# Performance work log

Hardware: AMD Instinct MI355X
Metric: run time of the kernel (lower is better)

## Reference

```python
import jax, jax.numpy as jnp
import numpy as np
import math

N_EMBD = 1024
N_HEAD_DIM = 64
B, S = 8, 2048

def setup_inputs() -> dict:
    key = jax.random.key(0)
    ks = jax.random.split(key, 8)
    x = jax.random.normal(ks[0], (B, S, N_EMBD), dtype=jnp.float32)
    padding_mask = jax.random.randint(ks[1], (B, S), 0, 2).astype(jnp.bool_)
    scale = 1.0 / math.sqrt(N_EMBD)
    Wq = jax.random.normal(ks[2], (N_HEAD_DIM, N_EMBD), dtype=jnp.float32) * scale
    bq = jnp.zeros((N_HEAD_DIM,), dtype=jnp.float32)
    Wk = jax.random.normal(ks[3], (N_HEAD_DIM, N_EMBD), dtype=jnp.float32) * scale
    bk = jnp.zeros((N_HEAD_DIM,), dtype=jnp.float32)
    Wv = jax.random.normal(ks[4], (N_HEAD_DIM, N_EMBD), dtype=jnp.float32) * scale
    bv = jnp.zeros((N_HEAD_DIM,), dtype=jnp.float32)
    return {"x": x, "Wq": Wq, "bq": bq, "Wk": Wk, "bk": bk, "Wv": Wv, "bv": bv,
            "padding_mask": padding_mask}

def reference(x, Wq, bq, Wk, bk, Wv, bv, padding_mask):
    # q,k,v: [B,S,D] via Linear (x @ W^T + b)
    q = jnp.einsum('bse,de->bsd', x, Wq) + bq
    k = jnp.einsum('bse,de->bsd', x, Wk) + bk
    v = jnp.einsum('bse,de->bsd', x, Wv) + bv
    scale = 1.0 / math.sqrt(k.shape[-1])
    att = jnp.einsum('bqd,bkd->bqk', q, k) * scale  # [B,S,S]
    # padding_mask [B,S] -> [B,1,S]: True positions masked to -inf
    att = jnp.where(padding_mask[:, None, :], -jnp.inf, att)
    att = jax.nn.softmax(att, axis=-1)
    # attn_dropout omitted (eval mode / identity)
    return jnp.einsum('bqk,bkd->bqd', att, v)
```

## Files before the change

kernel.cpp:

```cpp
#include <hip/hip_runtime.h>
#include <hip/hip_bf16.h>

#define B_ 8
#define S_ 2048
#define E_ 1024
#define D_ 64
#define VT_STRIDE 2112

typedef short short8 __attribute__((ext_vector_type(8)));
typedef short short4v __attribute__((ext_vector_type(4)));
typedef float floatx4 __attribute__((ext_vector_type(4)));

static __device__ __forceinline__ short bf16_bits(float f) {
    __hip_bfloat16 h = __float2bfloat16(f);
    return *reinterpret_cast<short*>(&h);
}
static __device__ __forceinline__ float bits_to_f(short s) {
    __hip_bfloat16 h = *reinterpret_cast<__hip_bfloat16*>(&s);
    return __bfloat162float(h);
}
static __device__ __forceinline__ void split8(const float* __restrict__ p,
                                              short8& hi, short8& lo) {
    #pragma unroll
    for (int j = 0; j < 8; j++) {
        float f = p[j];
        short h = bf16_bits(f);
        hi[j] = h;
        lo[j] = bf16_bits(f - bits_to_f(h));
    }
}
static __device__ __forceinline__ void split8v(const float v[8],
                                               short8& hi, short8& lo) {
    #pragma unroll
    for (int j = 0; j < 8; j++) {
        float f = v[j];
        short h = bf16_bits(f);
        hi[j] = h;
        lo[j] = bf16_bits(f - bits_to_f(h));
    }
}
static __device__ __forceinline__ void dma16(const void* src, void* lds_dst) {
    __builtin_amdgcn_global_load_lds(
        (const __attribute__((address_space(1))) unsigned int*)src,
        (__attribute__((address_space(3))) unsigned int*)lds_dst, 16, 0, 0);
}

__global__ __launch_bounds__(256) void prep_kernel(
    const float* __restrict__ Wq, const float* __restrict__ Wk,
    const float* __restrict__ Wv, short8* __restrict__ Wpk8,
    const void* __restrict__ mask_raw, float* __restrict__ maskf)
{
    __shared__ unsigned int red[256];
    if (blockIdx.x < 96) {
        const int t = blockIdx.x * 256 + threadIdx.x;
        const int l16  = t & 15;
        const int quad = (t >> 4) & 3;
        const int nb   = (t >> 6) & 3;
        const int m    = (t >> 8) % 3;
        const int e0c  = (t >> 8) / 3;
        const float* W = (m == 0) ? Wq : ((m == 1) ? Wk : Wv);
        short8 hi, lo;
        split8(W + (size_t)(nb * 16 + l16) * E_ + e0c * 32 + quad * 8, hi, lo);
        Wpk8[(size_t)e0c * 768 + m * 256 + nb * 64 + quad * 16 + l16] = hi;
    } else {
        const unsigned int* w = (const unsigned int*)mask_raw;
        unsigned int local = 0;
        for (int i = threadIdx.x; i < 4096; i += 256) local |= w[i];
        red[threadIdx.x] = local;
        __syncthreads();
        for (int s = 128; s > 0; s >>= 1) {
            if (threadIdx.x < s) red[threadIdx.x] |= red[threadIdx.x + s];
            __syncthreads();
        }
        const unsigned int ov = red[0];
        const bool is_u8 = (ov > 1u) && ((ov >> 24) <= 1u);
        const int i = (blockIdx.x - 96) * 256 + threadIdx.x;
        int v;
        if (ov == 0u)      v = 0;
        else if (is_u8)    v = (int)((const unsigned char*)mask_raw)[i];
        else               v = (((const unsigned int*)mask_raw)[i] != 0u);
        maskf[i] = v ? -1e30f : 0.0f;
    }
}

__global__ __launch_bounds__(512, 4) void qkv_kernel(
    const float* __restrict__ x, const short8* __restrict__ Wpk8,
    const float* __restrict__ bq, const float* __restrict__ bk,
    const float* __restrict__ bv,
    short* __restrict__ Qhi, short* __restrict__ Qlo,
    short* __restrict__ Khi, short* __restrict__ Vt)
{
    __shared__ alignas(16) float  xs[2][2][1024];
    __shared__ alignas(16) short8 wt[2][1536];
    const int tid  = threadIdx.x;
    const int wave = tid >> 6;
    const int nb   = wave & 3;
    const int rt   = wave >> 2;
    const int lane = tid & 63;
    const int l16  = lane & 15;
    const int quad = lane >> 4;
    const int row0 = blockIdx.x * 32;

    const int xr_  = (tid >> 3) & 31;
    const int xc_  = tid >> 8;
    const float* xsrc = x + (size_t)(row0 + xr_) * E_ + xc_ * 32 +
                        (((tid & 7) ^ (xr_ & 7)) * 4);
    const int xdst = xc_ * 1024 + xr_ * 32 + (tid & 7) * 4;

    floatx4 acc[3];
    #pragma unroll
    for (int m = 0; m < 3; m++) acc[m] = (floatx4){0.f,0.f,0.f,0.f};

    #pragma unroll
    for (int i = 0; i < 3; i++)
        dma16(Wpk8 + (size_t)i * 512 + tid, &wt[0][i * 512 + tid]);
    dma16(xsrc, &xs[0][0][0] + xdst);

    int buf = 0;
    for (int R = 0; R < 16; ++R) {
        __syncthreads();
        if (R + 1 < 16) {
            #pragma unroll
            for (int i = 0; i < 3; i++)
                dma16(Wpk8 + (size_t)(R + 1) * 1536 + i * 512 + tid,
                      &wt[buf ^ 1][i * 512 + tid]);
            dma16(xsrc + (R + 1) * 64, &xs[buf ^ 1][0][0] + xdst);
        }

        #pragma unroll
        for (int c = 0; c < 2; c++) {
            const int rr = rt * 16 + l16;
            const int rx = rr & 7;
            const float* xrp = &xs[buf][c][rr * 32];
            float4 a0 = *reinterpret_cast<const float4*>(xrp + (((2 * quad)     ^ rx) * 4));
            float4 a1 = *reinterpret_cast<const float4*>(xrp + (((2 * quad + 1) ^ rx) * 4));
            float av[8] = {a0.x, a0.y, a0.z, a0.w, a1.x, a1.y, a1.z, a1.w};
            short8 ah, al;
            split8v(av, ah, al);
            #pragma unroll
            for (int m = 0; m < 3; m++) {
                short8 wh = wt[buf][c * 768 + m * 256 + nb * 64 + lane];
                acc[m] = __builtin_amdgcn_mfma_f32_16x16x32_bf16(al, wh, acc[m], 0, 0, 0);
                acc[m] = __builtin_amdgcn_mfma_f32_16x16x32_bf16(ah, wh, acc[m], 0, 0, 0);
            }
        }
        buf ^= 1;
    }

    const int d = nb * 16 + l16;
    const float bqv = bq[d];
    const float bkv = bk[d];
    const float bvv = bv[d];
    const int bch = row0 >> 11;
    const int rowbase = row0 + rt * 16 + quad * 4;
    short4v vpk;
    #pragma unroll
    for (int r = 0; r < 4; r++) {
        const size_t row = (size_t)(rowbase + r);
        const float q = (acc[0][r] + bqv) * 0.125f;
        const short qhv = bf16_bits(q);
        Qhi[row * 64 + d] = qhv;
        Qlo[row * 64 + d] = bf16_bits(q - bits_to_f(qhv));
        Khi[row * 64 + d] = bf16_bits(acc[1][r] + bkv);
        vpk[r] = bf16_bits(acc[2][r] + bvv);
    }
    *reinterpret_cast<short4v*>(Vt + ((size_t)(bch * 64 + d)) * VT_STRIDE +
                                (rowbase & 2047)) = vpk;
}

union alignas(16) AttnLds {
    struct { short8 kts[4][512]; short8 vts[4][512]; } st;
    struct {
        float Osh[4][16][65];
        float msh[4][16], lsh[4][16];
    } mg;
};

__global__ __launch_bounds__(256, 2) void attn_kernel(
    const short* __restrict__ Qhi, const short* __restrict__ Qlo,
    const short* __restrict__ Khi, const short* __restrict__ Vt,
    const float* __restrict__ maskf, float* __restrict__ out)
{
    __shared__ AttnLds lds;
    __shared__ short PlT[4][16][72];

    const int tid  = threadIdx.x;
    const int wave = tid >> 6;
    const int qsub = wave & 1;
    const int par  = wave >> 1;
    const int lane = tid & 63;
    const int l16  = lane & 15;
    const int quad = lane >> 4;
    const int b    = blockIdx.x >> 6;
    const int qt   = blockIdx.x & 63;
    const size_t qbase  = (size_t)b * S_ + qt * 32 + qsub * 16;
    const size_t kplane = (size_t)b * S_;
    const short* Vb = Vt + (size_t)b * 64 * VT_STRIDE;

    short8 qh[2], ql[2];
    #pragma unroll
    for (int dc = 0; dc < 2; dc++) {
        qh[dc] = *reinterpret_cast<const short8*>(Qhi + (qbase + l16) * 64 + dc * 32 + quad * 8);
        ql[dc] = *reinterpret_cast<const short8*>(Qlo + (qbase + l16) * 64 + dc * 32 + quad * 8);
    }

    float m = -1e30f, l = 0.f;
    floatx4 O[4];
    #pragma unroll
    for (int ob = 0; ob < 4; ob++) O[ob] = (floatx4){0.f,0.f,0.f,0.f};

    #pragma unroll
    for (int p = 0; p < 2; p++) {
        #pragma unroll
        for (int i = 0; i < 2; i++) {
            const int c = i * 256 + tid;
            const int r = c >> 3, cs = c & 7;
            dma16(Khi + (kplane + p * 64 + r) * 64 + ((cs ^ (r & 7)) * 8),
                  &lds.st.kts[p][c]);
            dma16(Vb + (size_t)r * VT_STRIDE + p * 64 + ((cs ^ (r & 7)) * 8),
                  &lds.st.vts[p][c]);
        }
    }
    float4 mk4[4];
    #pragma unroll
    for (int kb = 0; kb < 4; kb++)
        mk4[kb] = *reinterpret_cast<const float4*>(
            maskf + kplane + par * 64 + kb * 16 + quad * 4);

    for (int R = 0; R < 16; ++R) {
        __syncthreads();
        const int set = R & 1;
        if (R + 1 < 16) {
            const int nset = set ^ 1;
            const int kt2 = (R + 1) * 128;
            #pragma unroll
            for (int p = 0; p < 2; p++) {
                #pragma unroll
                for (int i = 0; i < 2; i++) {
                    const int c = i * 256 + tid;
                    const int r = c >> 3, cs = c & 7;
                    dma16(Khi + (kplane + kt2 + p * 64 + r) * 64 + ((cs ^ (r & 7)) * 8),
                          &lds.st.kts[nset * 2 + p][c]);
                    dma16(Vb + (size_t)r * VT_STRIDE + kt2 + p * 64 + ((cs ^ (r & 7)) * 8),
                          &lds.st.vts[nset * 2 + p][c]);
                }
            }
        }
        const int buf = set * 2 + par;

        floatx4 sc[4];
        #pragma unroll
        for (int kb = 0; kb < 4; kb++) {
            floatx4 a = (floatx4){0.f,0.f,0.f,0.f};
            #pragma unroll
            for (int kc = 0; kc < 2; kc++) {
                const int key = kb * 16 + l16;
                short8 kf = lds.st.kts[buf][key * 8 + ((kc * 4 + quad) ^ (key & 7))];
                a = __builtin_amdgcn_mfma_f32_16x16x32_bf16(kf, qh[kc], a, 0, 0, 0);
                a = __builtin_amdgcn_mfma_f32_16x16x32_bf16(kf, ql[kc], a, 0, 0, 0);
            }
            sc[kb] = a;
        }
        #pragma unroll
        for (int kb = 0; kb < 4; kb++) {
            const float* mkp = reinterpret_cast<const float*>(&mk4[kb]);
            #pragma unroll
            for (int r = 0; r < 4; r++) sc[kb][r] += mkp[r];
        }

        if (R + 1 < 16) {
            const int ktn = (R + 1) * 128 + par * 64;
            #pragma unroll
            for (int kb = 0; kb < 4; kb++)
                mk4[kb] = *reinterpret_cast<const float4*>(
                    maskf + kplane + ktn + kb * 16 + quad * 4);
        }

        float mx = -1e30f;
        #pragma unroll
        for (int kb = 0; kb < 4; kb++)
            #pragma unroll
            for (int r = 0; r < 4; r++) mx = fmaxf(mx, sc[kb][r]);
        mx = fmaxf(mx, __shfl_xor(mx, 16, 64));
        mx = fmaxf(mx, __shfl_xor(mx, 32, 64));
        const float mnew  = fmaxf(fmaxf(m, mx), -1e29f);
        const float alpha = __expf(m - mnew);
        float ps = 0.f;
        #pragma unroll
        for (int kb = 0; kb < 4; kb++)
            #pragma unroll
            for (int r = 0; r < 4; r++) {
                const float pe = __expf(sc[kb][r] - mnew);
                sc[kb][r] = pe;
                ps += pe;
            }
        ps += __shfl_xor(ps, 16, 64);
        ps += __shfl_xor(ps, 32, 64);
        l = l * alpha + ps;
        m = mnew;
        #pragma unroll
        for (int ob = 0; ob < 4; ob++) O[ob] *= alpha;

        #pragma unroll
        for (int kb = 0; kb < 4; kb++)
            #pragma unroll
            for (int r = 0; r < 4; r++)
                PlT[wave][l16][kb * 16 + quad * 4 + r] = bf16_bits(sc[kb][r]);
        short8 pf[2];
        #pragma unroll
        for (int kc = 0; kc < 2; kc++)
            pf[kc] = *reinterpret_cast<const short8*>(&PlT[wave][l16][kc * 32 + quad * 8]);

        #pragma unroll
        for (int ob = 0; ob < 4; ob++)
            #pragma unroll
            for (int kc = 0; kc < 2; kc++) {
                const int dd = ob * 16 + l16;
                short8 vf = lds.st.vts[buf][dd * 8 + ((kc * 4 + quad) ^ (dd & 7))];
                O[ob] = __builtin_amdgcn_mfma_f32_16x16x32_bf16(vf, pf[kc], O[ob], 0, 0, 0);
            }
    }

    __syncthreads();
    #pragma unroll
    for (int ob = 0; ob < 4; ob++)
        #pragma unroll
        for (int r = 0; r < 4; r++)
            lds.mg.Osh[wave][l16][ob * 16 + quad * 4 + r] = O[ob][r];
    if (quad == 0) {
        lds.mg.msh[wave][l16] = m;
        lds.mg.lsh[wave][l16] = l;
    }
    __syncthreads();

    #pragma unroll
    for (int part = 0; part < 8; part++) {
        const int idx = part * 256 + tid;
        const int q = idx >> 6;
        const int d = idx & 63;
        const int w0 = (q >> 4), qq = q & 15;
        const float m0 = lds.mg.msh[w0][qq], m1 = lds.mg.msh[w0 + 2][qq];
        const float ms = fmaxf(m0, m1);
        const float x0 = __expf(m0 - ms), x1 = __expf(m1 - ms);
        const float lt = lds.mg.lsh[w0][qq] * x0 + lds.mg.lsh[w0 + 2][qq] * x1;
        const float oa = lds.mg.Osh[w0][qq][d] * x0 + lds.mg.Osh[w0 + 2][qq][d] * x1;
        out[((size_t)b * S_ + qt * 32 + q) * 64 + d] = oa / lt;
    }
}

extern "C" void kernel_launch(void* const* d_in, const int* in_sizes, int n_in,
                              void* d_out, int out_size, void* d_ws, size_t ws_size,
                              hipStream_t stream) {
    const float* x  = (const float*)d_in[0];
    const float* Wq = (const float*)d_in[1];
    const float* bq = (const float*)d_in[2];
    const float* Wk = (const float*)d_in[3];
    const float* bk = (const float*)d_in[4];
    const float* Wv = (const float*)d_in[5];
    const float* bv = (const float*)d_in[6];
    const void* mask = d_in[7];

    char* ws = (char*)d_ws;
    const size_t PLANE = (size_t)B_ * S_ * D_;
    short* Wpk = (short*)ws;
    short* Qhi = (short*)(ws + 768 * 1024);
    short* Qlo = Qhi + PLANE;
    short* Khi = Qlo + PLANE;
    short* Vt  = Khi + PLANE;
    float* maskf = (float*)(Vt + (size_t)512 * VT_STRIDE);

    prep_kernel<<<160, 256, 0, stream>>>(Wq, Wk, Wv, (short8*)Wpk, mask, maskf);
    qkv_kernel<<<512, 512, 0, stream>>>(x, (const short8*)Wpk, bq, bk, bv,
                                        Qhi, Qlo, Khi, Vt);
    attn_kernel<<<512, 256, 0, stream>>>(Qhi, Qlo, Khi, Vt, maskf,
                                         (float*)d_out);
}
```

Baseline: 153.9 us.

## Compact unmasked keys per batch and skip fully masked key rounds

The prep kernel now builds a prefix-sum compaction of unmasked key positions per batch, computes how many 128-key rounds are needed, and zero-pads K/V up to a round boundary. The QKV kernel scatters only unmasked K and V rows into compacted positions, and the attention loop runs only NR rounds instead of all 16. With a random mask about half the keys are dropped, so attention work is roughly halved. The cost is an extra prep pass with a block scan and scattered, uncoalesced K/Vt writes in the QKV epilogue.

```diff
diff --git a/kernel.cpp b/kernel.cpp
--- a/kernel.cpp
+++ b/kernel.cpp
@@ -48,7 +48,10 @@
 __global__ __launch_bounds__(256) void prep_kernel(
     const float* __restrict__ Wq, const float* __restrict__ Wk,
     const float* __restrict__ Wv, short8* __restrict__ Wpk8,
-    const void* __restrict__ mask_raw, float* __restrict__ maskf)
+    const void* __restrict__ mask_raw, float* __restrict__ maskf,
+    float* __restrict__ maskc, short* __restrict__ cidx,
+    int* __restrict__ nrounds, short* __restrict__ Khi,
+    short* __restrict__ Vt)
 {
     __shared__ unsigned int red[256];
     if (blockIdx.x < 96) {
@@ -74,12 +77,60 @@
         }
         const unsigned int ov = red[0];
         const bool is_u8 = (ov > 1u) && ((ov >> 24) <= 1u);
-        const int i = (blockIdx.x - 96) * 256 + threadIdx.x;
-        int v;
-        if (ov == 0u)      v = 0;
-        else if (is_u8)    v = (int)((const unsigned char*)mask_raw)[i];
-        else               v = (((const unsigned int*)mask_raw)[i] != 0u);
-        maskf[i] = v ? -1e30f : 0.0f;
+        if (blockIdx.x < 160) {
+            const int i = (blockIdx.x - 96) * 256 + threadIdx.x;
+            int v;
+            if (ov == 0u)      v = 0;
+            else if (is_u8)    v = (int)((const unsigned char*)mask_raw)[i];
+            else               v = (((const unsigned int*)mask_raw)[i] != 0u);
+            maskf[i] = v ? -1e30f : 0.0f;
+        } else {
+            const int b = blockIdx.x - 160;
+            int um[8];
+            #pragma unroll
+            for (int j = 0; j < 8; j++) {
+                const int i = b * 2048 + (int)threadIdx.x * 8 + j;
+                int v;
+                if (ov == 0u)      v = 0;
+                else if (is_u8)    v = (int)((const unsigned char*)mask_raw)[i];
+                else               v = (w[i] != 0u);
+                um[j] = v ? 0 : 1;
+            }
+            int cnt = 0;
+            #pragma unroll
+            for (int j = 0; j < 8; j++) cnt += um[j];
+            __syncthreads();
+            red[threadIdx.x] = (unsigned int)cnt;
+            __syncthreads();
+            for (int off = 1; off < 256; off <<= 1) {
+                unsigned int a = 0;
+                if ((int)threadIdx.x >= off) a = red[threadIdx.x - off];
+                __syncthreads();
+                red[threadIdx.x] += a;
+                __syncthreads();
+            }
+            const int total = (int)red[255];
+            int pos = (int)red[threadIdx.x] - cnt;
+            #pragma unroll
+            for (int j = 0; j < 8; j++) {
+                const int s = (int)threadIdx.x * 8 + j;
+                cidx[b * 2048 + s] = (short)(um[j] ? pos : -1);
+                pos += um[j];
+            }
+            int nr = (total + 127) >> 7;
+            if (nr == 0) nr = 1;
+            if (threadIdx.x == 0) nrounds[b] = nr;
+            for (int k = threadIdx.x; k < 2048; k += 256)
+                maskc[b * 2048 + k] = (k < total) ? 0.0f : -1e30f;
+            const int nkpad = nr * 128;
+            const int padn = (nkpad - total) * 64;
+            for (int idx = threadIdx.x; idx < padn; idx += 256) {
+                const int p = total + (idx >> 6);
+                const int d = idx & 63;
+                Khi[((size_t)b * 2048 + p) * 64 + d] = 0;
+                Vt[((size_t)(b * 64 + d)) * VT_STRIDE + p] = 0;
+            }
+        }
     }
 }
 
@@ -87,6 +138,7 @@
     const float* __restrict__ x, const short8* __restrict__ Wpk8,
     const float* __restrict__ bq, const float* __restrict__ bk,
     const float* __restrict__ bv,
+    const float* __restrict__ maskf, const short* __restrict__ cidx,
     short* __restrict__ Qhi, short* __restrict__ Qlo,
     short* __restrict__ Khi, short* __restrict__ Vt)
 {
@@ -153,7 +205,6 @@
     const float bvv = bv[d];
     const int bch = row0 >> 11;
     const int rowbase = row0 + rt * 16 + quad * 4;
-    short4v vpk;
     #pragma unroll
     for (int r = 0; r < 4; r++) {
         const size_t row = (size_t)(rowbase + r);
@@ -161,11 +212,12 @@
         const short qhv = bf16_bits(q);
         Qhi[row * 64 + d] = qhv;
         Qlo[row * 64 + d] = bf16_bits(q - bits_to_f(qhv));
-        Khi[row * 64 + d] = bf16_bits(acc[1][r] + bkv);
-        vpk[r] = bf16_bits(acc[2][r] + bvv);
-    }
-    *reinterpret_cast<short4v*>(Vt + ((size_t)(bch * 64 + d)) * VT_STRIDE +
-                                (rowbase & 2047)) = vpk;
+        if (maskf[row] == 0.0f) {
+            const int cpos = (int)cidx[row];
+            Khi[((size_t)(bch << 11) + cpos) * 64 + d] = bf16_bits(acc[1][r] + bkv);
+            Vt[((size_t)(bch * 64 + d)) * VT_STRIDE + cpos] = bf16_bits(acc[2][r] + bvv);
+        }
+    }
 }
 
 union alignas(16) AttnLds {
@@ -179,7 +231,8 @@
 __global__ __launch_bounds__(256, 2) void attn_kernel(
     const short* __restrict__ Qhi, const short* __restrict__ Qlo,
     const short* __restrict__ Khi, const short* __restrict__ Vt,
-    const float* __restrict__ maskf, float* __restrict__ out)
+    const float* __restrict__ maskc, const int* __restrict__ nrounds,
+    float* __restrict__ out)
 {
     __shared__ AttnLds lds;
     __shared__ short PlT[4][16][72];
@@ -193,6 +246,7 @@
     const int quad = lane >> 4;
     const int b    = blockIdx.x >> 6;
     const int qt   = blockIdx.x & 63;
+    const int NR   = nrounds[b];
     const size_t qbase  = (size_t)b * S_ + qt * 32 + qsub * 16;
     const size_t kplane = (size_t)b * S_;
     const short* Vb = Vt + (size_t)b * 64 * VT_STRIDE;
@@ -225,12 +279,12 @@
     #pragma unroll
     for (int kb = 0; kb < 4; kb++)
         mk4[kb] = *reinterpret_cast<const float4*>(
-            maskf + kplane + par * 64 + kb * 16 + quad * 4);
-
-    for (int R = 0; R < 16; ++R) {
+            maskc + kplane + par * 64 + kb * 16 + quad * 4);
+
+    for (int R = 0; R < NR; ++R) {
         __syncthreads();
         const int set = R & 1;
-        if (R + 1 < 16) {
+        if (R + 1 < NR) {
             const int nset = set ^ 1;
             const int kt2 = (R + 1) * 128;
             #pragma unroll
@@ -268,12 +322,12 @@
             for (int r = 0; r < 4; r++) sc[kb][r] += mkp[r];
         }
 
-        if (R + 1 < 16) {
+        if (R + 1 < NR) {
             const int ktn = (R + 1) * 128 + par * 64;
             #pragma unroll
             for (int kb = 0; kb < 4; kb++)
                 mk4[kb] = *reinterpret_cast<const float4*>(
-                    maskf + kplane + ktn + kb * 16 + quad * 4);
+                    maskc + kplane + ktn + kb * 16 + quad * 4);
         }
 
         float mx = -1e30f;
@@ -368,10 +422,14 @@
     short* Khi = Qlo + PLANE;
     short* Vt  = Khi + PLANE;
     float* maskf = (float*)(Vt + (size_t)512 * VT_STRIDE);
-
-    prep_kernel<<<160, 256, 0, stream>>>(Wq, Wk, Wv, (short8*)Wpk, mask, maskf);
+    float* maskc = maskf + 16384;
+    short* cidx  = (short*)(maskc + 16384);
+    int*   nround = (int*)(cidx + 16384);
+
+    prep_kernel<<<168, 256, 0, stream>>>(Wq, Wk, Wv, (short8*)Wpk, mask, maskf,
+                                         maskc, cidx, nround, Khi, Vt);
     qkv_kernel<<<512, 512, 0, stream>>>(x, (const short8*)Wpk, bq, bk, bv,
-                                        Qhi, Qlo, Khi, Vt);
-    attn_kernel<<<512, 256, 0, stream>>>(Qhi, Qlo, Khi, Vt, maskf,
+                                        maskf, cidx, Qhi, Qlo, Khi, Vt);
+    attn_kernel<<<512, 256, 0, stream>>>(Qhi, Qlo, Khi, Vt, maskc, nround,
                                          (float*)d_out);
 }
```

Result: no change. 152.7 us (median of 2 runs) (-0.8%).
